# Optimization experiments

Hardware: AMD Instinct MI355X
Metric: run time of the kernel (lower is better)

The kernel has to match this reference:

```python
import jax, jax.numpy as jnp
import numpy as np

T, B, C, H, W = 4, 8, 256, 16, 16
HEADS = 8
N = H * W
TN = T * N
DH = C // HEADS
DECAY = 0.25

# STE quantizer: fwd round(clamp(x,0,1)); bwd passes grad only where 0<=x<=1
@jax.custom_vjp
def quant1(x):
    return jnp.round(jnp.clip(x, 0.0, 1.0))

def _q_fwd(x):
    return quant1(x), x

def _q_bwd(x, g):
    return (jnp.where((x < 0) | (x > 1), 0.0, g),)

quant1.defvjp(_q_fwd, _q_bwd)

def lif(x):
    # x: [T, ...]; sequential LIF membrane decay + quantize over leading (time) axis
    def step(carry, xt):
        mem_old, spike = carry
        mem = (mem_old - jax.lax.stop_gradient(spike) * 0.5) * DECAY + xt
        s = quant1(mem)
        return (mem, s), s
    z = jnp.zeros_like(x[0])
    _, out = jax.lax.scan(step, (z, z), x)
    return out

def bn1d(x, gamma, beta, mean, var):
    # eval-mode BatchNorm1d over channel axis 1 of [B, Ch, L]
    inv = jax.lax.rsqrt(var + 1e-5)
    return (x - mean[None, :, None]) * (gamma * inv)[None, :, None] + beta[None, :, None]

def _rel_pos_index():
    coords = np.stack(np.meshgrid(np.arange(T), np.arange(H), np.arange(W), indexing='ij'))  # [3,T,H,W]
    cf = coords.reshape(3, -1)                      # [3, TN]
    rc = (cf[:, :, None] - cf[:, None, :]).transpose(1, 2, 0).copy()  # [TN, TN, 3]
    rc[:, :, 0] += T - 1
    rc[:, :, 1] += H - 1
    rc[:, :, 2] += W - 1
    rc[:, :, 0] *= (2 * H - 1) * (2 * W - 1)
    rc[:, :, 1] *= (2 * W - 1)
    return rc.sum(-1)                               # [TN, TN] ints

def _mask():
    m = np.ones((TN, TN), np.float32)
    for t in range(T - 1):
        m[t * N:(t + 1) * N, (t + 1) * N:] = 0.0
    return m

_RPI = jnp.asarray(_rel_pos_index().reshape(-1))
_MASK = jnp.asarray(_mask())


def setup_inputs() -> dict:
    key = jax.random.key(0)
    ks = jax.random.split(key, 13)
    bias_rows = (2 * T - 1) * (2 * H - 1) * (2 * W - 1)
    return {
        'x': jax.random.normal(ks[0], (T, B, C, H, W), jnp.float32),
        'w_qkv': jax.random.normal(ks[1], (3 * C, C), jnp.float32) * 0.05,
        'qkv_gamma': jax.random.uniform(ks[2], (3 * C,), jnp.float32, 0.5, 1.5),
        'qkv_beta': jax.random.normal(ks[3], (3 * C,), jnp.float32) * 0.1,
        'qkv_mean': jax.random.normal(ks[4], (3 * C,), jnp.float32) * 0.1,
        'qkv_var': jax.random.uniform(ks[5], (3 * C,), jnp.float32, 0.5, 1.5),
        'bias_table': jax.random.normal(ks[6], (bias_rows, HEADS), jnp.float32) * 0.02,
        'w_proj': jax.random.normal(ks[7], (C, C), jnp.float32) * 0.05,
        'b_proj': jax.random.normal(ks[8], (C,), jnp.float32) * 0.02,
        'proj_gamma': jax.random.uniform(ks[9], (C,), jnp.float32, 0.5, 1.5),
        'proj_beta': jax.random.normal(ks[10], (C,), jnp.float32) * 0.1,
        'proj_mean': jax.random.normal(ks[11], (C,), jnp.float32) * 0.1,
        'proj_var': jax.random.uniform(ks[12], (C,), jnp.float32, 0.5, 1.5),
    }


def reference(x, w_qkv, qkv_gamma, qkv_beta, qkv_mean, qkv_var, bias_table,
              w_proj, b_proj, proj_gamma, proj_beta, proj_mean, proj_var):
    # flatten spatial, then raw reshape [T,B,C,N] -> [B,C,T*N] (as in torch source)
    xf = x.reshape(T, B, C, N).reshape(B, C, T * N)
    # 1x1 conv == channel matmul, then eval BN
    qkv = jnp.einsum('oc,bcl->bol', w_qkv, xf)
    qkv = bn1d(qkv, qkv_gamma, qkv_beta, qkv_mean, qkv_var)
    qkv = qkv.reshape(B, 3 * C, T, N).transpose(2, 0, 1, 3)  # [T,B,3C,N]
    qkv = lif(qkv).transpose(1, 0, 3, 2)                      # [B,T,N,3C]
    q, k, v = jnp.split(qkv, 3, axis=-1)                      # each [B,T,N,C]

    def to_heads(z):  # b t n (h d) -> b h (t n) d
        return z.reshape(B, T, N, HEADS, DH).transpose(0, 3, 1, 2, 4).reshape(B, HEADS, TN, DH)
    q, k, v = map(to_heads, (q, k, v))

    bias = bias_table[_RPI].reshape(TN, TN, HEADS).transpose(2, 0, 1)  # [h,TN,TN]
    attn = jnp.einsum('bhnd,bhmd->bhnm', q, k) + bias[None]
    attn = attn * _MASK[None, None]                                     # block upper-triangle mask
    o = jnp.einsum('bhnm,bhmd->bhnd', attn, v) * 0.125                  # [B,h,TN,d]

    o = o.transpose(0, 2, 1, 3).reshape(B, TN, C).reshape(B, T, N, C).transpose(1, 0, 3, 2)  # [T,B,C,N]
    o = lif(o)
    o = o.transpose(1, 2, 0, 3).reshape(B, C, T * N)          # [B,C,TN]
    o = jnp.einsum('oc,bcl->bol', w_proj, o) + b_proj[None, :, None]
    o = bn1d(o, proj_gamma, proj_beta, proj_mean, proj_var)
    o = o.reshape(B, C, T, N).transpose(2, 0, 1, 3).reshape(T, B, C, H, W)
    return lif(o)
```

## Files before the change

kernel.cpp:

```cpp
#include <hip/hip_runtime.h>
#include <stdint.h>
#include <math.h>

constexpr int T_ = 4;
constexpr int B_ = 8;
constexpr int C_ = 256;
constexpr int N_ = 256;
constexpr int TN_ = 1024;
constexpr int NH_ = 8;
constexpr int O3_ = 768;
constexpr int BIAS_ROWS_ = 6727;

__device__ __constant__ int TI_OF[10] = {0,1,1,2,2,2,3,3,3,3};
__device__ __constant__ int TJ_OF[10] = {0,0,1,0,1,2,0,1,2,3};

__device__ __forceinline__ float quant1f(float m) {
    return rintf(fminf(fmaxf(m, 0.0f), 1.0f));
}

__global__ __launch_bounds__(256) void k1_qkv_lif(
    const float* __restrict__ x, const float* __restrict__ w,
    const float* __restrict__ gamma, const float* __restrict__ beta,
    const float* __restrict__ mean, const float* __restrict__ var,
    uint32_t* __restrict__ qb, uint32_t* __restrict__ kb, uint32_t* __restrict__ vb)
{
    __shared__ float At[32][68];
    __shared__ float Bt[32][132];
    const int b = blockIdx.z;
    const int oBase = blockIdx.y * 64;
    const int nBase = blockIdx.x * 32;
    const int tid = threadIdx.x;
    const float* xb = x + (size_t)b * C_ * TN_;

    const int tyc = tid >> 5;
    const int txc = tid & 31;

    const int a_row0 = tid >> 4;
    const int a_k2 = (tid & 15) * 2;
    const int b_n = tid & 31;
    const int b_kk0 = tid >> 5;

    float acc[8][4];
#pragma unroll
    for (int i = 0; i < 8; ++i)
#pragma unroll
        for (int j = 0; j < 4; ++j) acc[i][j] = 0.0f;

    for (int kc = 0; kc < 8; ++kc) {
        const int k0 = kc * 32;
#pragma unroll
        for (int r = 0; r < 4; ++r) {
            const int row = a_row0 + 16 * r;
            const float2 v = *(const float2*)&w[(size_t)(oBase + row) * C_ + k0 + a_k2];
            At[a_k2][row] = v.x;
            At[a_k2 + 1][row] = v.y;
        }
#pragma unroll
        for (int r = 0; r < 4; ++r) {
            const int kk = b_kk0 + 8 * r;
            const float* src = &xb[(size_t)(k0 + kk) * TN_ + nBase + b_n];
            float4 v;
            v.x = src[0];
            v.y = src[256];
            v.z = src[512];
            v.w = src[768];
            *(float4*)&Bt[kk][b_n * 4] = v;
        }
        __syncthreads();
#pragma unroll
        for (int cc = 0; cc < 32; ++cc) {
            float a[8], bb[4];
            *(float4*)&a[0] = *(const float4*)&At[cc][tyc * 8];
            *(float4*)&a[4] = *(const float4*)&At[cc][tyc * 8 + 4];
            *(float4*)&bb[0] = *(const float4*)&Bt[cc][txc * 4];
#pragma unroll
            for (int i = 0; i < 8; ++i)
#pragma unroll
                for (int j = 0; j < 4; ++j) acc[i][j] += a[i] * bb[j];
        }
        __syncthreads();
    }

    const int o0 = oBase + tyc * 8;
    const int which = o0 >> 8;
    const int h = (o0 >> 5) & 7;
    const int dq = tyc & 3;
    const int n = nBase + txc;
    uint8_t* dst = (uint8_t*)((which == 0) ? qb : (which == 1) ? kb : vb);

    uint32_t bits[4] = {0u, 0u, 0u, 0u};
#pragma unroll
    for (int i = 0; i < 8; ++i) {
        const int o = o0 + i;
        const float inv = 1.0f / sqrtf(var[o] + 1e-5f);
        const float g = gamma[o] * inv;
        const float mn = mean[o], bt = beta[o];
        float memv = 0.0f, spk = 0.0f;
#pragma unroll
        for (int t = 0; t < 4; ++t) {
            const float val = (acc[i][t] - mn) * g + bt;
            const float m = (memv - 0.5f * spk) * 0.25f + val;
            memv = m;
            const float s = quant1f(m);
            spk = s;
            bits[t] |= ((uint32_t)s) << i;
        }
    }
#pragma unroll
    for (int t = 0; t < 4; ++t)
        dst[4 * (((size_t)b * NH_ + h) * TN_ + t * N_ + n) + dq] = (uint8_t)bits[t];
}

__global__ __launch_bounds__(256) void k3_tgp(
    const uint32_t* __restrict__ kb, const uint32_t* __restrict__ vb,
    int* __restrict__ Pt)
{
    __shared__ uint64_t ks[32][4];
    __shared__ uint64_t vs[32][4];
    const int t = blockIdx.x;
    const int bh = blockIdx.y;
    const int tid = threadIdx.x;
    const int q = tid >> 6, lane = tid & 63;
    const int j = t * N_ + q * 64 + lane;

    const uint32_t kw = kb[(size_t)bh * TN_ + j];
    const uint32_t vw = vb[(size_t)bh * TN_ + j];
#pragma unroll
    for (int d = 0; d < 32; ++d) {
        const uint64_t mk = __ballot((kw >> d) & 1u);
        const uint64_t mv = __ballot((vw >> d) & 1u);
        if (lane == 0) { ks[d][q] = mk; vs[d][q] = mv; }
    }
    __syncthreads();

    const int d = tid & 31;
#pragma unroll
    for (int s = 0; s < 4; ++s) {
        const int d2 = (tid >> 5) + 8 * s;
        int p = 0;
#pragma unroll
        for (int w = 0; w < 4; ++w) p += __popcll(ks[d2][w] & vs[d][w]);
        Pt[(size_t)(bh * 4 + t) * 1024 + d2 * 32 + d] = p;
    }
}

__global__ __launch_bounds__(256) void k3_cum(
    const int* __restrict__ Pt, float* __restrict__ Gf)
{
    const int bh = blockIdx.x;
    const int tid = threadIdx.x;
#pragma unroll
    for (int r = 0; r < 4; ++r) {
        const int idx = tid + 256 * r;
        int cum = 0;
#pragma unroll
        for (int t = 0; t < T_; ++t) {
            cum += Pt[(size_t)(bh * 4 + t) * 1024 + idx];
            Gf[(size_t)(bh * 4 + t) * 1024 + idx] = (float)cum;
        }
    }
}

__global__ __launch_bounds__(256) void k3_bias_gemm(
    const uint32_t* __restrict__ vb, const float* __restrict__ bias_table,
    float* __restrict__ p0, float* __restrict__ p1,
    float* __restrict__ p2, float* __restrict__ p3)
{
    __shared__ float sbl[544];
    __shared__ float At[32][36];
    __shared__ float Bt[32][132];

    const int z = blockIdx.z;
    const int h = z / 10;
    const int p = z % 10;
    const int ti = TI_OF[p], tj = TJ_OF[p];
    const int dt = ti - tj;
    const int iT = blockIdx.y;
    const int nBase = blockIdx.x * 128;
    const int tid = threadIdx.x;

    const int base = 3363 + 961 * dt + 62 * iT - 480;
    for (int s = tid; s < 544; s += 256) {
        const int gidx = base + s;
        sbl[s] = (gidx >= 0 && gidx < BIAS_ROWS_) ? bias_table[(size_t)gidx * NH_ + h] : 0.0f;
    }

    const int ty2 = tid >> 4, tx16 = tid & 15;

    const int il0 = ty2 * 2;
    const int sRowBase = 480 + 31 * (il0 >> 4) + (il0 & 15) - tx16;

    const int n8 = tx16 * 8;
    const int nS = nBase + n8;
    const int bS = nS >> 5, d0S = nS & 31;
    const uint32_t* vbw = vb + ((size_t)bS * NH_ + h) * TN_ + tj * 256 + ty2;

    const int tyc = tid >> 5, txc = tid & 31;
    const int nA = nBase + txc * 4;
    const int bA = nA >> 5, dA = nA & 31;

    float acc[4][4];
#pragma unroll
    for (int i = 0; i < 4; ++i)
#pragma unroll
        for (int j = 0; j < 4; ++j) acc[i][j] = 0.0f;

    __syncthreads();

    for (int kc = 0; kc < 8; ++kc) {
#pragma unroll
        for (int r1 = 0; r1 < 2; ++r1) {
            const int s0 = sRowBase - 31 * (kc * 2 + r1);
            float2 av;
            av.x = sbl[s0];
            av.y = sbl[s0 + 1];
            At[tx16 + 16 * r1][il0] = av.x;
            At[tx16 + 16 * r1][il0 + 1] = av.y;
        }
#pragma unroll
        for (int r = 0; r < 2; ++r) {
            const uint32_t wd = vbw[kc * 32 + 16 * r];
            float4 b0, b1;
            b0.x = (float)((wd >> d0S) & 1u);
            b0.y = (float)((wd >> (d0S + 1)) & 1u);
            b0.z = (float)((wd >> (d0S + 2)) & 1u);
            b0.w = (float)((wd >> (d0S + 3)) & 1u);
            b1.x = (float)((wd >> (d0S + 4)) & 1u);
            b1.y = (float)((wd >> (d0S + 5)) & 1u);
            b1.z = (float)((wd >> (d0S + 6)) & 1u);
            b1.w = (float)((wd >> (d0S + 7)) & 1u);
            *(float4*)&Bt[ty2 + 16 * r][n8] = b0;
            *(float4*)&Bt[ty2 + 16 * r][n8 + 4] = b1;
        }
        __syncthreads();
#pragma unroll
        for (int cc = 0; cc < 32; ++cc) {
            float a[4], bb[4];
            *(float4*)&a[0] = *(const float4*)&At[cc][tyc * 4];
            *(float4*)&bb[0] = *(const float4*)&Bt[cc][txc * 4];
#pragma unroll
            for (int i = 0; i < 4; ++i)
#pragma unroll
                for (int j = 0; j < 4; ++j) acc[i][j] += a[i] * bb[j];
        }
        __syncthreads();
    }

    float* plane = (tj == 0) ? p0 : (tj == 1) ? p1 : (tj == 2) ? p2 : p3;
    const int nrows = (4 - tj) * 256;
    const int cA = h * 32 + dA;
#pragma unroll
    for (int r = 0; r < 4; ++r) {
        const int rowL = dt * 256 + iT * 32 + tyc * 4 + r;
        float4 s0;
        s0.x = acc[r][0]; s0.y = acc[r][1]; s0.z = acc[r][2]; s0.w = acc[r][3];
        *(float4*)&plane[((size_t)bA * nrows + rowL) * 256 + cA] = s0;
    }
}

__global__ __launch_bounds__(256) void k4_lif2(
    const uint32_t* __restrict__ qb, const float* __restrict__ Gf,
    const float* __restrict__ p0, const float* __restrict__ p1,
    const float* __restrict__ p2, const float* __restrict__ p3,
    uint32_t* __restrict__ s2c)
{
    const int c = threadIdx.x;
    const int n = blockIdx.x;
    const int b = blockIdx.y;
    const int lane = c & 63;
    const int h = c >> 5, d = c & 31;
    const int bh = b * NH_ + h;
    const uint32_t* qbh = qb + (size_t)bh * TN_;

    float memv = 0.0f, spk = 0.0f;
    for (int t = 0; t < T_; ++t) {
        const int l = t * N_ + n;
        const uint32_t q = qbh[l];
        const float* g = Gf + (size_t)(bh * 4 + t) * 1024 + d;
        float v = 0.0f;
#pragma unroll
        for (int d2 = 0; d2 < 32; ++d2)
            v += ((q >> d2) & 1u) ? g[d2 * 32] : 0.0f;
        v += p0[((size_t)b * 1024 + l) * 256 + c];
        if (t >= 1) v += p1[((size_t)b * 768 + (l - 256)) * 256 + c];
        if (t >= 2) v += p2[((size_t)b * 512 + (l - 512)) * 256 + c];
        if (t >= 3) v += p3[((size_t)b * 256 + (l - 768)) * 256 + c];
        const float m = (memv - 0.5f * spk) * 0.25f + 0.125f * v;
        memv = m;
        const float s = quant1f(m);
        spk = s;
        const uint64_t mask = __ballot(s != 0.0f);
        if (lane == 0)
            s2c[((size_t)b * TN_ + l) * 8 + (c >> 5)] = (uint32_t)mask;
        else if (lane == 32)
            s2c[((size_t)b * TN_ + l) * 8 + (c >> 5)] = (uint32_t)(mask >> 32);
    }
}

__global__ __launch_bounds__(256) void k5_proj_lif(
    const uint32_t* __restrict__ s2c, const float* __restrict__ w,
    const float* __restrict__ bp,
    const float* __restrict__ gamma, const float* __restrict__ beta,
    const float* __restrict__ mean, const float* __restrict__ var,
    float* __restrict__ out)
{
    __shared__ float At[128][36];
    __shared__ uint32_t Sw[128 * 9];
    const int nBase = blockIdx.x * 32;
    const int oBase = blockIdx.y * 32;
    const int b = blockIdx.z;
    const int tid = threadIdx.x;
    const int tx = tid & 31;
    const int ty = tid >> 5;

#pragma unroll
    for (int j = 0; j < 4; ++j) {
        const int fidx = tid * 4 + j;
        const int lp = fidx >> 3, wsel = fidx & 7;
        const int t = lp >> 5, nn = lp & 31;
        Sw[lp * 9 + wsel] = s2c[((size_t)b * TN_ + t * 256 + nBase + nn) * 8 + wsel];
    }

    const int a_row = tid >> 3, a_kq = (tid & 7) * 16;

    float acc[4][4];
#pragma unroll
    for (int r = 0; r < 4; ++r)
#pragma unroll
        for (int t = 0; t < 4; ++t) acc[r][t] = 0.0f;

    for (int half = 0; half < 2; ++half) {
        if (half) __syncthreads();
#pragma unroll
        for (int j = 0; j < 4; ++j) {
            const float4 v = *(const float4*)&w[(size_t)(oBase + a_row) * C_ + half * 128 + a_kq + 4 * j];
            At[a_kq + 4 * j][a_row] = v.x;
            At[a_kq + 4 * j + 1][a_row] = v.y;
            At[a_kq + 4 * j + 2][a_row] = v.z;
            At[a_kq + 4 * j + 3][a_row] = v.w;
        }
        __syncthreads();

        for (int ks = 0; ks < 4; ++ks) {
            uint32_t wr[4];
#pragma unroll
            for (int t = 0; t < 4; ++t)
                wr[t] = Sw[(t * 32 + tx) * 9 + half * 4 + ks];
#pragma unroll
            for (int u = 0; u < 32; ++u) {
                float a[4];
                *(float4*)&a[0] = *(const float4*)&At[ks * 32 + u][ty * 4];
                float bv[4];
#pragma unroll
                for (int t = 0; t < 4; ++t) bv[t] = (float)((wr[t] >> u) & 1u);
#pragma unroll
                for (int r = 0; r < 4; ++r)
#pragma unroll
                    for (int t = 0; t < 4; ++t) acc[r][t] += a[r] * bv[t];
            }
        }
    }

#pragma unroll
    for (int r = 0; r < 4; ++r) {
        const int o = oBase + ty * 4 + r;
        const float inv = 1.0f / sqrtf(var[o] + 1e-5f);
        const float g = gamma[o] * inv;
        const float mn = mean[o], bt = beta[o], bpo = bp[o];
        float memv = 0.0f, spk = 0.0f;
#pragma unroll
        for (int t = 0; t < 4; ++t) {
            const float val = ((acc[r][t] + bpo) - mn) * g + bt;
            const float m = (memv - 0.5f * spk) * 0.25f + val;
            memv = m;
            const float s = quant1f(m);
            spk = s;
            out[(((size_t)t * B_ + b) * C_ + o) * N_ + nBase + tx] = s;
        }
    }
}

extern "C" void kernel_launch(void* const* d_in, const int* in_sizes, int n_in,
                              void* d_out, int out_size, void* d_ws, size_t ws_size,
                              hipStream_t stream)
{
    const float* x          = (const float*)d_in[0];
    const float* w_qkv      = (const float*)d_in[1];
    const float* qkv_gamma  = (const float*)d_in[2];
    const float* qkv_beta   = (const float*)d_in[3];
    const float* qkv_mean   = (const float*)d_in[4];
    const float* qkv_var    = (const float*)d_in[5];
    const float* bias_table = (const float*)d_in[6];
    const float* w_proj     = (const float*)d_in[7];
    const float* b_proj     = (const float*)d_in[8];
    const float* proj_gamma = (const float*)d_in[9];
    const float* proj_beta  = (const float*)d_in[10];
    const float* proj_mean  = (const float*)d_in[11];
    const float* proj_var   = (const float*)d_in[12];
    float* out = (float*)d_out;

    char* ws = (char*)d_ws;
    float*    part0  = (float*)(ws + 1048576);
    float*    part1  = (float*)(ws + 9437184);
    float*    part2  = (float*)(ws + 15728640);
    float*    part3  = (float*)(ws + 19922944);
    float*    Gf     = (float*)(ws + 25165824);
    int*      Pt     = (int*)  (ws + 26214400);
    uint32_t* s2c    = (uint32_t*)(ws + 33554432);
    uint32_t* qbits  = (uint32_t*)(ws + 50331648);
    uint32_t* kbits  = (uint32_t*)(ws + 50593792);
    uint32_t* vbits  = (uint32_t*)(ws + 50855936);

    k1_qkv_lif<<<dim3(8, 12, 8), 256, 0, stream>>>(
        x, w_qkv, qkv_gamma, qkv_beta, qkv_mean, qkv_var, qbits, kbits, vbits);

    k3_tgp<<<dim3(4, 64), 256, 0, stream>>>(kbits, vbits, Pt);

    k3_cum<<<dim3(64), 256, 0, stream>>>(Pt, Gf);

    k3_bias_gemm<<<dim3(2, 8, 80), 256, 0, stream>>>(
        vbits, bias_table, part0, part1, part2, part3);

    k4_lif2<<<dim3(256, 8), 256, 0, stream>>>(
        qbits, Gf, part0, part1, part2, part3, s2c);

    k5_proj_lif<<<dim3(8, 8, 8), 256, 0, stream>>>(
        s2c, w_proj, b_proj, proj_gamma, proj_beta, proj_mean, proj_var, out);
}
```

Baseline: 207.3 us.

## Fuse gram and prefix-sum kernels, enlarge bias GEMM tile, reuse G rows

Merges the per-timestep K^T V popcount kernel with the cumulative-sum kernel into a single kernel that loops over time and keeps running sums in registers, removing one launch and the Pt round trip. The bias GEMM now runs 128 threads per block, each computing an 8x4 output tile instead of 4x4, for more register reuse per shared load. The second LIF kernel handles two spatial positions per block and loads the G column into registers once per timestep for both. The trade-offs are fewer blocks and threads in flight (64 blocks for the fused gram kernel) and higher register pressure in the GEMM and LIF kernels.

```diff
diff --git a/kernel.cpp b/kernel.cpp
--- a/kernel.cpp
+++ b/kernel.cpp
@@ -111,57 +111,44 @@
         dst[4 * (((size_t)b * NH_ + h) * TN_ + t * N_ + n) + dq] = (uint8_t)bits[t];
 }
 
-__global__ __launch_bounds__(256) void k3_tgp(
+__global__ __launch_bounds__(256) void k3_gram(
     const uint32_t* __restrict__ kb, const uint32_t* __restrict__ vb,
-    int* __restrict__ Pt)
+    float* __restrict__ Gf)
 {
     __shared__ uint64_t ks[32][4];
     __shared__ uint64_t vs[32][4];
-    const int t = blockIdx.x;
-    const int bh = blockIdx.y;
+    const int bh = blockIdx.x;
     const int tid = threadIdx.x;
     const int q = tid >> 6, lane = tid & 63;
-    const int j = t * N_ + q * 64 + lane;
-
-    const uint32_t kw = kb[(size_t)bh * TN_ + j];
-    const uint32_t vw = vb[(size_t)bh * TN_ + j];
-#pragma unroll
-    for (int d = 0; d < 32; ++d) {
-        const uint64_t mk = __ballot((kw >> d) & 1u);
-        const uint64_t mv = __ballot((vw >> d) & 1u);
-        if (lane == 0) { ks[d][q] = mk; vs[d][q] = mv; }
-    }
-    __syncthreads();
-
     const int d = tid & 31;
-#pragma unroll
-    for (int s = 0; s < 4; ++s) {
-        const int d2 = (tid >> 5) + 8 * s;
-        int p = 0;
-#pragma unroll
-        for (int w = 0; w < 4; ++w) p += __popcll(ks[d2][w] & vs[d][w]);
-        Pt[(size_t)(bh * 4 + t) * 1024 + d2 * 32 + d] = p;
-    }
-}
-
-__global__ __launch_bounds__(256) void k3_cum(
-    const int* __restrict__ Pt, float* __restrict__ Gf)
-{
-    const int bh = blockIdx.x;
-    const int tid = threadIdx.x;
-#pragma unroll
-    for (int r = 0; r < 4; ++r) {
-        const int idx = tid + 256 * r;
-        int cum = 0;
-#pragma unroll
-        for (int t = 0; t < T_; ++t) {
-            cum += Pt[(size_t)(bh * 4 + t) * 1024 + idx];
-            Gf[(size_t)(bh * 4 + t) * 1024 + idx] = (float)cum;
-        }
-    }
-}
-
-__global__ __launch_bounds__(256) void k3_bias_gemm(
+
+    int cum[4] = {0, 0, 0, 0};
+
+    for (int t = 0; t < T_; ++t) {
+        const int j = t * N_ + tid;
+        const uint32_t kw = kb[(size_t)bh * TN_ + j];
+        const uint32_t vw = vb[(size_t)bh * TN_ + j];
+#pragma unroll
+        for (int dd = 0; dd < 32; ++dd) {
+            const uint64_t mk = __ballot((kw >> dd) & 1u);
+            const uint64_t mv = __ballot((vw >> dd) & 1u);
+            if (lane == 0) { ks[dd][q] = mk; vs[dd][q] = mv; }
+        }
+        __syncthreads();
+#pragma unroll
+        for (int s = 0; s < 4; ++s) {
+            const int d2 = (tid >> 5) + 8 * s;
+            int p = 0;
+#pragma unroll
+            for (int w = 0; w < 4; ++w) p += __popcll(ks[d2][w] & vs[d][w]);
+            cum[s] += p;
+            Gf[(size_t)(bh * 4 + t) * 1024 + tid + 256 * s] = (float)cum[s];
+        }
+        __syncthreads();
+    }
+}
+
+__global__ __launch_bounds__(128) void k3_bias_gemm(
     const uint32_t* __restrict__ vb, const float* __restrict__ bias_table,
     float* __restrict__ p0, float* __restrict__ p1,
     float* __restrict__ p2, float* __restrict__ p3)
@@ -180,14 +167,14 @@
     const int tid = threadIdx.x;
 
     const int base = 3363 + 961 * dt + 62 * iT - 480;
-    for (int s = tid; s < 544; s += 256) {
+    for (int s = tid; s < 544; s += 128) {
         const int gidx = base + s;
         sbl[s] = (gidx >= 0 && gidx < BIAS_ROWS_) ? bias_table[(size_t)gidx * NH_ + h] : 0.0f;
     }
 
     const int ty2 = tid >> 4, tx16 = tid & 15;
 
-    const int il0 = ty2 * 2;
+    const int il0 = ty2 * 4;
     const int sRowBase = 480 + 31 * (il0 >> 4) + (il0 & 15) - tx16;
 
     const int n8 = tx16 * 8;
@@ -199,9 +186,9 @@
     const int nA = nBase + txc * 4;
     const int bA = nA >> 5, dA = nA & 31;
 
-    float acc[4][4];
-#pragma unroll
-    for (int i = 0; i < 4; ++i)
+    float acc[8][4];
+#pragma unroll
+    for (int i = 0; i < 8; ++i)
 #pragma unroll
         for (int j = 0; j < 4; ++j) acc[i][j] = 0.0f;
 
@@ -211,15 +198,14 @@
 #pragma unroll
         for (int r1 = 0; r1 < 2; ++r1) {
             const int s0 = sRowBase - 31 * (kc * 2 + r1);
-            float2 av;
-            av.x = sbl[s0];
-            av.y = sbl[s0 + 1];
-            At[tx16 + 16 * r1][il0] = av.x;
-            At[tx16 + 16 * r1][il0 + 1] = av.y;
-        }
-#pragma unroll
-        for (int r = 0; r < 2; ++r) {
-            const uint32_t wd = vbw[kc * 32 + 16 * r];
+            const int cc = tx16 + 16 * r1;
+#pragma unroll
+            for (int rr = 0; rr < 4; ++rr)
+                At[cc][il0 + rr] = sbl[s0 + rr];
+        }
+#pragma unroll
+        for (int r = 0; r < 4; ++r) {
+            const uint32_t wd = vbw[kc * 32 + 8 * r];
             float4 b0, b1;
             b0.x = (float)((wd >> d0S) & 1u);
             b0.y = (float)((wd >> (d0S + 1)) & 1u);
@@ -229,17 +215,18 @@
             b1.y = (float)((wd >> (d0S + 5)) & 1u);
             b1.z = (float)((wd >> (d0S + 6)) & 1u);
             b1.w = (float)((wd >> (d0S + 7)) & 1u);
-            *(float4*)&Bt[ty2 + 16 * r][n8] = b0;
-            *(float4*)&Bt[ty2 + 16 * r][n8 + 4] = b1;
+            *(float4*)&Bt[ty2 + 8 * r][n8] = b0;
+            *(float4*)&Bt[ty2 + 8 * r][n8 + 4] = b1;
         }
         __syncthreads();
 #pragma unroll
         for (int cc = 0; cc < 32; ++cc) {
-            float a[4], bb[4];
-            *(float4*)&a[0] = *(const float4*)&At[cc][tyc * 4];
+            float a[8], bb[4];
+            *(float4*)&a[0] = *(const float4*)&At[cc][tyc * 8];
+            *(float4*)&a[4] = *(const float4*)&At[cc][tyc * 8 + 4];
             *(float4*)&bb[0] = *(const float4*)&Bt[cc][txc * 4];
 #pragma unroll
-            for (int i = 0; i < 4; ++i)
+            for (int i = 0; i < 8; ++i)
 #pragma unroll
                 for (int j = 0; j < 4; ++j) acc[i][j] += a[i] * bb[j];
         }
@@ -250,8 +237,8 @@
     const int nrows = (4 - tj) * 256;
     const int cA = h * 32 + dA;
 #pragma unroll
-    for (int r = 0; r < 4; ++r) {
-        const int rowL = dt * 256 + iT * 32 + tyc * 4 + r;
+    for (int r = 0; r < 8; ++r) {
+        const int rowL = dt * 256 + iT * 32 + tyc * 8 + r;
         float4 s0;
         s0.x = acc[r][0]; s0.y = acc[r][1]; s0.z = acc[r][2]; s0.w = acc[r][3];
         *(float4*)&plane[((size_t)bA * nrows + rowL) * 256 + cA] = s0;
@@ -265,35 +252,41 @@
     uint32_t* __restrict__ s2c)
 {
     const int c = threadIdx.x;
-    const int n = blockIdx.x;
+    const int n0 = blockIdx.x * 2;
     const int b = blockIdx.y;
     const int lane = c & 63;
     const int h = c >> 5, d = c & 31;
     const int bh = b * NH_ + h;
     const uint32_t* qbh = qb + (size_t)bh * TN_;
 
-    float memv = 0.0f, spk = 0.0f;
+    float memv[2] = {0.0f, 0.0f}, spk[2] = {0.0f, 0.0f};
     for (int t = 0; t < T_; ++t) {
-        const int l = t * N_ + n;
-        const uint32_t q = qbh[l];
         const float* g = Gf + (size_t)(bh * 4 + t) * 1024 + d;
-        float v = 0.0f;
-#pragma unroll
-        for (int d2 = 0; d2 < 32; ++d2)
-            v += ((q >> d2) & 1u) ? g[d2 * 32] : 0.0f;
-        v += p0[((size_t)b * 1024 + l) * 256 + c];
-        if (t >= 1) v += p1[((size_t)b * 768 + (l - 256)) * 256 + c];
-        if (t >= 2) v += p2[((size_t)b * 512 + (l - 512)) * 256 + c];
-        if (t >= 3) v += p3[((size_t)b * 256 + (l - 768)) * 256 + c];
-        const float m = (memv - 0.5f * spk) * 0.25f + 0.125f * v;
-        memv = m;
-        const float s = quant1f(m);
-        spk = s;
-        const uint64_t mask = __ballot(s != 0.0f);
-        if (lane == 0)
-            s2c[((size_t)b * TN_ + l) * 8 + (c >> 5)] = (uint32_t)mask;
-        else if (lane == 32)
-            s2c[((size_t)b * TN_ + l) * 8 + (c >> 5)] = (uint32_t)(mask >> 32);
+        float gv[32];
+#pragma unroll
+        for (int d2 = 0; d2 < 32; ++d2) gv[d2] = g[d2 * 32];
+#pragma unroll
+        for (int j = 0; j < 2; ++j) {
+            const int l = t * N_ + n0 + j;
+            const uint32_t q = qbh[l];
+            float v = 0.0f;
+#pragma unroll
+            for (int d2 = 0; d2 < 32; ++d2)
+                v += ((q >> d2) & 1u) ? gv[d2] : 0.0f;
+            v += p0[((size_t)b * 1024 + l) * 256 + c];
+            if (t >= 1) v += p1[((size_t)b * 768 + (l - 256)) * 256 + c];
+            if (t >= 2) v += p2[((size_t)b * 512 + (l - 512)) * 256 + c];
+            if (t >= 3) v += p3[((size_t)b * 256 + (l - 768)) * 256 + c];
+            const float m = (memv[j] - 0.5f * spk[j]) * 0.25f + 0.125f * v;
+            memv[j] = m;
+            const float s = quant1f(m);
+            spk[j] = s;
+            const uint64_t mask = __ballot(s != 0.0f);
+            if (lane == 0)
+                s2c[((size_t)b * TN_ + l) * 8 + (c >> 5)] = (uint32_t)mask;
+            else if (lane == 32)
+                s2c[((size_t)b * TN_ + l) * 8 + (c >> 5)] = (uint32_t)(mask >> 32);
+        }
     }
 }
 
@@ -405,7 +398,6 @@
     float*    part2  = (float*)(ws + 15728640);
     float*    part3  = (float*)(ws + 19922944);
     float*    Gf     = (float*)(ws + 25165824);
-    int*      Pt     = (int*)  (ws + 26214400);
     uint32_t* s2c    = (uint32_t*)(ws + 33554432);
     uint32_t* qbits  = (uint32_t*)(ws + 50331648);
     uint32_t* kbits  = (uint32_t*)(ws + 50593792);
@@ -414,14 +406,12 @@
     k1_qkv_lif<<<dim3(8, 12, 8), 256, 0, stream>>>(
         x, w_qkv, qkv_gamma, qkv_beta, qkv_mean, qkv_var, qbits, kbits, vbits);
 
-    k3_tgp<<<dim3(4, 64), 256, 0, stream>>>(kbits, vbits, Pt);
-
-    k3_cum<<<dim3(64), 256, 0, stream>>>(Pt, Gf);
-
-    k3_bias_gemm<<<dim3(2, 8, 80), 256, 0, stream>>>(
+    k3_gram<<<dim3(64), 256, 0, stream>>>(kbits, vbits, Gf);
+
+    k3_bias_gemm<<<dim3(2, 8, 80), 128, 0, stream>>>(
         vbits, bias_table, part0, part1, part2, part3);
 
-    k4_lif2<<<dim3(256, 8), 256, 0, stream>>>(
+    k4_lif2<<<dim3(128, 8), 256, 0, stream>>>(
         qbits, Gf, part0, part1, part2, part3, s2c);
 
     k5_proj_lif<<<dim3(8, 8, 8), 256, 0, stream>>>(
```

Result: slower. 213.2 us (+2.9%).
